# Performance work log

Measured on AMD Instinct MI355X. Metric: run time of the kernel, lower is better.

## Reference

```python
import jax, jax.numpy as jnp
import numpy as np

N = 100000
E = 1600000
IN_FEATS = 512
H1, F1 = 8, 8          # layer1: 8 heads x 8 units
H2, F2 = 1, 40         # layer2: 1 head x out_feats
NEG_SLOPE = 0.2


def setup_inputs() -> dict:
    key = jax.random.key(0)
    ks = jax.random.split(key, 12)
    x = jax.random.normal(ks[0], (N, IN_FEATS), dtype=jnp.float32)
    src = jax.random.randint(ks[1], (E,), 0, N, dtype=jnp.int32)
    dst = jax.random.randint(ks[2], (E,), 0, N, dtype=jnp.int32)
    # Xavier-ish init for params
    W1 = jax.random.normal(ks[3], (IN_FEATS, H1 * F1), dtype=jnp.float32) * (1.0 / np.sqrt(IN_FEATS))
    al1 = jax.random.normal(ks[4], (H1, F1), dtype=jnp.float32) * 0.1
    ar1 = jax.random.normal(ks[5], (H1, F1), dtype=jnp.float32) * 0.1
    b1 = jnp.zeros((H1 * F1,), dtype=jnp.float32)
    W2 = jax.random.normal(ks[6], (H1 * F1, H2 * F2), dtype=jnp.float32) * (1.0 / np.sqrt(H1 * F1))
    al2 = jax.random.normal(ks[7], (H2, F2), dtype=jnp.float32) * 0.1
    ar2 = jax.random.normal(ks[8], (H2, F2), dtype=jnp.float32) * 0.1
    b2 = jnp.zeros((H2 * F2,), dtype=jnp.float32)
    return {"x": x, "src": src, "dst": dst,
            "W1": W1, "al1": al1, "ar1": ar1, "b1": b1,
            "W2": W2, "al2": al2, "ar2": ar2, "b2": b2}


def _gat_conv(feat, src, dst, W, al, ar, b, activation):
    """DGL-style GATConv (dropout disabled / eval mode)."""
    n = feat.shape[0]
    heads, fdim = al.shape
    h = (feat @ W).reshape(n, heads, fdim)            # [N, H, F]
    el = jnp.einsum('nhf,hf->nh', h, al)              # [N, H]
    er = jnp.einsum('nhf,hf->nh', h, ar)              # [N, H]
    e = jax.nn.leaky_relu(el[src] + er[dst], NEG_SLOPE)   # [E, H]
    # edge softmax over incoming edges of each dst node (numerically stable)
    m = jax.ops.segment_max(e, dst, num_segments=n)   # [N, H]
    ex = jnp.exp(e - m[dst])
    s = jax.ops.segment_sum(ex, dst, num_segments=n)  # [N, H]
    alpha = ex / s[dst]                               # [E, H]
    msg = h[src] * alpha[:, :, None]                  # [E, H, F]
    rst = jax.ops.segment_sum(msg, dst, num_segments=n)  # [N, H, F]
    rst = rst + b.reshape(1, heads, fdim)
    if activation is not None:
        rst = activation(rst)
    return rst


def reference(x, src, dst, W1, al1, ar1, b1, W2, al2, ar2, b2):
    h1 = _gat_conv(x, src, dst, W1, al1, ar1, b1, jax.nn.elu)   # [N, H1, F1]
    h1 = h1.reshape(x.shape[0], H1 * F1)                        # flatten(1)
    h2 = _gat_conv(h1, src, dst, W2, al2, ar2, b2, None)        # [N, 1, F2]
    logits = h2.mean(axis=1)                                    # [N, F2]
    return jax.nn.log_softmax(logits, axis=1)
```

## Files before the change

kernel.cpp:

```cpp
#include <hip/hip_runtime.h>
#include <cstdint>
#include <cstddef>

#define IN_F 512
#define C1 64
#define NH 8
#define FD 8
#define C2 40
#define NEG 0.2f

typedef __attribute__((ext_vector_type(8))) short bf16x8;
typedef __attribute__((ext_vector_type(4))) float f32x4;

__device__ inline unsigned short f32_to_bf16_rne(float f) {
    unsigned int u = __float_as_uint(f);
    unsigned int r = (u + 0x7FFFu + ((u >> 16) & 1u)) >> 16;
    return (unsigned short)r;
}
__device__ inline float bf16_to_f32(unsigned short s) {
    return __uint_as_float(((unsigned int)s) << 16);
}

__global__ __launch_bounds__(256) void hist_k(const int* __restrict__ dst, int* __restrict__ deg,
                                              int* __restrict__ pos, int E) {
    int e = blockIdx.x * 256 + threadIdx.x;
    if (e < E) pos[e] = atomicAdd(&deg[dst[e]], 1);
}

__global__ __launch_bounds__(1024) void scan_local_k(const int* __restrict__ deg, int* __restrict__ rowp,
                                                     int* __restrict__ bsums, int n) {
    __shared__ int tmp[1024];
    int tx = threadIdx.x;
    int i = blockIdx.x * 1024 + tx;
    int v = (i < n) ? deg[i] : 0;
    tmp[tx] = v;
    __syncthreads();
    for (int d = 1; d < 1024; d <<= 1) {
        int t = (tx >= d) ? tmp[tx - d] : 0;
        __syncthreads();
        tmp[tx] += t;
        __syncthreads();
    }
    if (i < n) rowp[i] = tmp[tx] - v;
    if (tx == 1023) bsums[blockIdx.x] = tmp[tx];
}

__global__ __launch_bounds__(128) void scan_sums_k(int* bsums, int nb) {
    __shared__ int tmp[128];
    int tx = threadIdx.x;
    int v = (tx < nb) ? bsums[tx] : 0;
    tmp[tx] = v;
    __syncthreads();
    for (int d = 1; d < 128; d <<= 1) {
        int t = (tx >= d) ? tmp[tx - d] : 0;
        __syncthreads();
        tmp[tx] += t;
        __syncthreads();
    }
    if (tx < nb) bsums[tx] = tmp[tx] - v;
}

__global__ __launch_bounds__(1024) void scan_add_k(int* rowp, const int* __restrict__ bsums, int n) {
    int i = blockIdx.x * 1024 + threadIdx.x;
    if (i < n) rowp[i] += bsums[blockIdx.x];
}

__global__ __launch_bounds__(256) void scatter_k(const int* __restrict__ src, const int* __restrict__ dst,
                                                 const int* __restrict__ rowp, const int* __restrict__ pos,
                                                 int* __restrict__ csr_src, int E) {
    int e = blockIdx.x * 256 + threadIdx.x;
    if (e >= E) return;
    csr_src[rowp[dst[e]] + pos[e]] = src[e];
}

__global__ __launch_bounds__(256) void wt_pre_k(const float* __restrict__ W1,
                                                unsigned short* __restrict__ wt_hi,
                                                unsigned short* __restrict__ wt_lo) {
    int id = blockIdx.x * 256 + threadIdx.x;
    if (id >= IN_F * C1) return;
    int col = id & (C1 - 1);
    int k = id >> 6;
    float w = W1[id];
    unsigned short hb = f32_to_bf16_rne(w);
    unsigned short lb = f32_to_bf16_rne(w - bf16_to_f32(hb));
    wt_hi[(size_t)col * IN_F + k] = hb;
    wt_lo[(size_t)col * IN_F + k] = lb;
}

__global__ __launch_bounds__(256) void gemm1_mfma_k(const float* __restrict__ x,
                                                    const unsigned short* __restrict__ wt_hi,
                                                    const unsigned short* __restrict__ wt_lo,
                                                    unsigned short* __restrict__ hb_out, int N) {
    __shared__ alignas(16) unsigned short wlds[2][8192];
    const int tid = threadIdx.x;
    const int wave = tid >> 6, lane = tid & 63;
    const int m = lane & 15, q = lane >> 4;
    const int row = blockIdx.x * 64 + wave * 16 + m;
    const int row_c = row < N ? row : N - 1;
    const float* xp = x + (size_t)row_c * IN_F + q * 8;

    f32x4 acc[4];
#pragma unroll
    for (int ct = 0; ct < 4; ct++) acc[ct] = (f32x4){0.f, 0.f, 0.f, 0.f};
    float4 xr[2][4];

#define WLOAD(c, buf)                                                                              \
    {                                                                                              \
        _Pragma("unroll") for (int j_ = 0; j_ < 4; j_++) {                                         \
            int slot_ = j_ * 256 + wave * 64 + lane;                                               \
            const unsigned short* gbase_ = (slot_ < 512) ? wt_hi : wt_lo;                          \
            int s_ = slot_ & 511;                                                                  \
            int col_ = s_ & 63, kq_ = s_ >> 6;                                                     \
            const unsigned short* g_ = gbase_ + (size_t)col_ * IN_F + (c) * 64 + kq_ * 8;          \
            unsigned short* l_ = &wlds[buf][0] + (size_t)(j_ * 256 + wave * 64) * 8;               \
            __builtin_amdgcn_global_load_lds((const __attribute__((address_space(1))) unsigned int*)g_, \
                                             (__attribute__((address_space(3))) unsigned int*)l_,  \
                                             16, 0, 0);                                            \
        }                                                                                          \
    }
#define XLOAD(c, r)                                  \
    {                                                \
        const float* xsrc_ = xp + (c) * 64;          \
        (r)[0] = *(const float4*)(xsrc_);            \
        (r)[1] = *(const float4*)(xsrc_ + 4);        \
        (r)[2] = *(const float4*)(xsrc_ + 32);       \
        (r)[3] = *(const float4*)(xsrc_ + 36);       \
    }

    WLOAD(0, 0);
    XLOAD(0, xr[0]);

    for (int c = 0; c < 8; c++) {
        int p = c & 1;
        __syncthreads();
        if (c < 7) {
            WLOAD(c + 1, p ^ 1);
            XLOAD(c + 1, xr[p ^ 1]);
        }
#pragma unroll
        for (int ki = 0; ki < 2; ki++) {
            float f[8];
            f[0] = xr[p][ki * 2].x; f[1] = xr[p][ki * 2].y; f[2] = xr[p][ki * 2].z; f[3] = xr[p][ki * 2].w;
            f[4] = xr[p][ki * 2 + 1].x; f[5] = xr[p][ki * 2 + 1].y; f[6] = xr[p][ki * 2 + 1].z; f[7] = xr[p][ki * 2 + 1].w;
            unsigned int u[8], lu[8];
#pragma unroll
            for (int j = 0; j < 8; j++) u[j] = __float_as_uint(f[j]);
            union { uint4 u4; bf16x8 v; } H, L;
            H.u4.x = __builtin_amdgcn_perm(u[1], u[0], 0x07060302u);
            H.u4.y = __builtin_amdgcn_perm(u[3], u[2], 0x07060302u);
            H.u4.z = __builtin_amdgcn_perm(u[5], u[4], 0x07060302u);
            H.u4.w = __builtin_amdgcn_perm(u[7], u[6], 0x07060302u);
#pragma unroll
            for (int j = 0; j < 8; j++)
                lu[j] = __float_as_uint(f[j] - __uint_as_float(u[j] & 0xFFFF0000u));
            L.u4.x = __builtin_amdgcn_perm(lu[1], lu[0], 0x07060302u);
            L.u4.y = __builtin_amdgcn_perm(lu[3], lu[2], 0x07060302u);
            L.u4.z = __builtin_amdgcn_perm(lu[5], lu[4], 0x07060302u);
            L.u4.w = __builtin_amdgcn_perm(lu[7], lu[6], 0x07060302u);
            int kq = ki * 4 + q;
#pragma unroll
            for (int ct = 0; ct < 4; ct++) {
                int slot = kq * 64 + ct * 16 + m;
                bf16x8 bh = *(const bf16x8*)&wlds[p][slot * 8];
                bf16x8 bl = *(const bf16x8*)&wlds[p][4096 + slot * 8];
                acc[ct] = __builtin_amdgcn_mfma_f32_16x16x32_bf16(H.v, bh, acc[ct], 0, 0, 0);
                acc[ct] = __builtin_amdgcn_mfma_f32_16x16x32_bf16(L.v, bh, acc[ct], 0, 0, 0);
                acc[ct] = __builtin_amdgcn_mfma_f32_16x16x32_bf16(H.v, bl, acc[ct], 0, 0, 0);
            }
        }
    }
    int rbase = blockIdx.x * 64 + wave * 16 + q * 4;
#pragma unroll
    for (int r = 0; r < 4; r++) {
        int ro = rbase + r;
        if (ro < N) {
#pragma unroll
            for (int ct = 0; ct < 4; ct++)
                hb_out[(size_t)ro * C1 + ct * 16 + m] = f32_to_bf16_rne(acc[ct][r]);
        }
    }
#undef WLOAD
#undef XLOAD
}

__global__ __launch_bounds__(256) void attn1_k(const unsigned short* __restrict__ hb,
                                               const float* __restrict__ al, const float* __restrict__ ar,
                                               float* __restrict__ el, float* __restrict__ er, int N) {
    int idx = blockIdx.x * 256 + threadIdx.x;
    if (idx >= N * NH) return;
    int n = idx >> 3, hd = idx & 7;
    bf16x8 v = *(const bf16x8*)(hb + (size_t)n * C1 + hd * FD);
    const float4* alp = (const float4*)(al + hd * FD);
    const float4* arp = (const float4*)(ar + hd * FD);
    float4 a0 = alp[0], a1 = alp[1];
    float4 r0 = arp[0], r1 = arp[1];
    float f[8];
#pragma unroll
    for (int j = 0; j < 8; j++) f[j] = bf16_to_f32((unsigned short)v[j]);
    float e_l = f[0] * a0.x + f[1] * a0.y + f[2] * a0.z + f[3] * a0.w +
                f[4] * a1.x + f[5] * a1.y + f[6] * a1.z + f[7] * a1.w;
    float e_r = f[0] * r0.x + f[1] * r0.y + f[2] * r0.z + f[3] * r0.w +
                f[4] * r1.x + f[5] * r1.y + f[6] * r1.z + f[7] * r1.w;
    el[idx] = e_l;
    er[idx] = e_r;
}

__global__ __launch_bounds__(256) void l1_wave_k(const unsigned short* __restrict__ hb,
                                                 const float* __restrict__ el, const float* __restrict__ er,
                                                 const int* __restrict__ rowp, const int* __restrict__ deg,
                                                 const int* __restrict__ csr_src, const float* __restrict__ b1,
                                                 float* __restrict__ h1out, int N) {
    int n = (blockIdx.x * 256 + threadIdx.x) >> 6;
    if (n >= N) return;
    int lane = threadIdx.x & 63;
    int hg = lane >> 3;
    int start = rowp[n], cnt = deg[n];
    float erd = er[n * NH + hg];
    float acc = 0.f, s = 0.f;
    int i = 0;
    for (; i + 4 <= cnt; i += 4) {
        const int* cp = csr_src + start + i;
        int sn0 = cp[0], sn1 = cp[1], sn2 = cp[2], sn3 = cp[3];
        float e0 = el[sn0 * NH + hg];
        float e1 = el[sn1 * NH + hg];
        float e2 = el[sn2 * NH + hg];
        float e3 = el[sn3 * NH + hg];
        unsigned short q0 = hb[(size_t)sn0 * C1 + lane];
        unsigned short q1 = hb[(size_t)sn1 * C1 + lane];
        unsigned short q2 = hb[(size_t)sn2 * C1 + lane];
        unsigned short q3 = hb[(size_t)sn3 * C1 + lane];
        e0 += erd; e1 += erd; e2 += erd; e3 += erd;
        e0 = e0 > 0.f ? e0 : NEG * e0;
        e1 = e1 > 0.f ? e1 : NEG * e1;
        e2 = e2 > 0.f ? e2 : NEG * e2;
        e3 = e3 > 0.f ? e3 : NEG * e3;
        float w0 = __expf(e0), w1 = __expf(e1), w2 = __expf(e2), w3 = __expf(e3);
        s += (w0 + w1) + (w2 + w3);
        acc += w0 * bf16_to_f32(q0) + w1 * bf16_to_f32(q1) + w2 * bf16_to_f32(q2) + w3 * bf16_to_f32(q3);
    }
    for (; i < cnt; i++) {
        int sn = csr_src[start + i];
        float e = el[sn * NH + hg] + erd;
        e = e > 0.f ? e : NEG * e;
        float w0 = __expf(e);
        s += w0;
        acc += w0 * bf16_to_f32(hb[(size_t)sn * C1 + lane]);
    }
    float sinv = (s > 0.f) ? 1.f / s : 0.f;
    float o = acc * sinv + b1[lane];
    o = o > 0.f ? o : (__expf(o) - 1.f);
    h1out[(size_t)n * C1 + lane] = o;
}

__global__ __launch_bounds__(256) void gemm2_attn2_k(const float* __restrict__ h1, const float* __restrict__ W2,
                                                     const float* __restrict__ al2, const float* __restrict__ ar2,
                                                     unsigned short* __restrict__ h2b, float* __restrict__ el2,
                                                     float* __restrict__ er2, int N) {
    __shared__ float ws[C1 * C2];
    __shared__ float hs[64][C1];
    __shared__ float h2s[64][C2];
    __shared__ float a2s[2 * C2];
    int t = threadIdx.x;
    int n0 = blockIdx.x * 64;
    for (int i = t; i < C1 * C2; i += 256) ws[i] = W2[i];
    if (t < C2) a2s[t] = al2[t];
    else if (t < 2 * C2) a2s[t] = ar2[t - C2];
    for (int i = t; i < 64 * 16; i += 256) {
        int r = i >> 4, c4 = i & 15;
        int n = n0 + r;
        float4 v = (n < N) ? *(const float4*)(h1 + (size_t)n * C1 + c4 * 4) : make_float4(0.f, 0.f, 0.f, 0.f);
        *(float4*)&hs[r][c4 * 4] = v;
    }
    __syncthreads();
    for (int o = t; o < 64 * C2; o += 256) {
        int r = o / C2, c = o % C2;
        float sum = 0.f;
#pragma unroll
        for (int k = 0; k < C1; k++) sum += hs[r][k] * ws[k * C2 + c];
        h2s[r][c] = sum;
    }
    __syncthreads();
    for (int o = t; o < 64 * 64; o += 256) {
        int r = o >> 6, c = o & 63;
        int nn = n0 + r;
        if (nn < N) h2b[(size_t)nn * 64 + c] = (c < C2) ? f32_to_bf16_rne(h2s[r][c]) : (unsigned short)0;
    }
    if (t < 64) {
        int nn = n0 + t;
        if (nn < N) {
            float e_l = 0.f, e_r = 0.f;
#pragma unroll
            for (int c = 0; c < C2; c++) {
                float v = h2s[t][c];
                e_l += v * a2s[c];
                e_r += v * a2s[C2 + c];
            }
            el2[nn] = e_l;
            er2[nn] = e_r;
        }
    }
}

__global__ __launch_bounds__(256) void l2_fused_k(const unsigned short* __restrict__ h2b,
                                                  const float* __restrict__ el, const float* __restrict__ er,
                                                  const int* __restrict__ rowp, const int* __restrict__ deg,
                                                  const int* __restrict__ csr_src, const float* __restrict__ b2,
                                                  float* __restrict__ out, int N) {
    int tid = threadIdx.x;
    int n = blockIdx.x * 32 + (tid >> 3);
    int sub = tid & 7;
    if (n >= N) return;
    int start = rowp[n], cnt = deg[n];
    float erd = er[n];
    float s = 0.f;
    float acc[8];
#pragma unroll
    for (int j = 0; j < 8; j++) acc[j] = 0.f;
    int i = 0;
    for (; i + 4 <= cnt; i += 4) {
        const int* cp = csr_src + start + i;
        int sn0 = cp[0], sn1 = cp[1], sn2 = cp[2], sn3 = cp[3];
        float e0 = el[sn0], e1 = el[sn1], e2 = el[sn2], e3 = el[sn3];
        bf16x8 v0 = *(const bf16x8*)(h2b + (size_t)sn0 * 64 + sub * 8);
        bf16x8 v1 = *(const bf16x8*)(h2b + (size_t)sn1 * 64 + sub * 8);
        bf16x8 v2 = *(const bf16x8*)(h2b + (size_t)sn2 * 64 + sub * 8);
        bf16x8 v3 = *(const bf16x8*)(h2b + (size_t)sn3 * 64 + sub * 8);
        e0 += erd; e1 += erd; e2 += erd; e3 += erd;
        e0 = e0 > 0.f ? e0 : NEG * e0;
        e1 = e1 > 0.f ? e1 : NEG * e1;
        e2 = e2 > 0.f ? e2 : NEG * e2;
        e3 = e3 > 0.f ? e3 : NEG * e3;
        float w0 = __expf(e0), w1 = __expf(e1), w2 = __expf(e2), w3 = __expf(e3);
        s += (w0 + w1) + (w2 + w3);
#pragma unroll
        for (int j = 0; j < 8; j++) {
            acc[j] += w0 * bf16_to_f32((unsigned short)v0[j]) + w1 * bf16_to_f32((unsigned short)v1[j]) +
                      w2 * bf16_to_f32((unsigned short)v2[j]) + w3 * bf16_to_f32((unsigned short)v3[j]);
        }
    }
    for (; i < cnt; i++) {
        int sn = csr_src[start + i];
        float e = el[sn] + erd;
        e = e > 0.f ? e : NEG * e;
        float w0 = __expf(e);
        s += w0;
        bf16x8 v = *(const bf16x8*)(h2b + (size_t)sn * 64 + sub * 8);
#pragma unroll
        for (int j = 0; j < 8; j++) acc[j] += w0 * bf16_to_f32((unsigned short)v[j]);
    }
    float sinv = (s > 0.f) ? 1.f / s : 0.f;
    float vals[8];
#pragma unroll
    for (int j = 0; j < 8; j++) {
        int c = sub * 8 + j;
        vals[j] = (c < C2) ? (acc[j] * sinv + b2[c]) : -1e30f;
    }
    float mx = vals[0];
#pragma unroll
    for (int j = 1; j < 8; j++) mx = fmaxf(mx, vals[j]);
#pragma unroll
    for (int off = 1; off < 8; off <<= 1) mx = fmaxf(mx, __shfl_xor(mx, off, 8));
    float se = 0.f;
#pragma unroll
    for (int j = 0; j < 8; j++) se += __expf(vals[j] - mx);
#pragma unroll
    for (int off = 1; off < 8; off <<= 1) se += __shfl_xor(se, off, 8);
    float ls = __logf(se) + mx;
    if (sub < 5) {
        float* op = out + (size_t)n * C2 + sub * 8;
        *(float4*)(op) = make_float4(vals[0] - ls, vals[1] - ls, vals[2] - ls, vals[3] - ls);
        *(float4*)(op + 4) = make_float4(vals[4] - ls, vals[5] - ls, vals[6] - ls, vals[7] - ls);
    }
}

extern "C" void kernel_launch(void* const* d_in, const int* in_sizes, int n_in,
                              void* d_out, int out_size, void* d_ws, size_t ws_size,
                              hipStream_t stream) {
    (void)n_in; (void)out_size; (void)ws_size;
    const float* x   = (const float*)d_in[0];
    const int*   src = (const int*)d_in[1];
    const int*   dst = (const int*)d_in[2];
    const float* W1  = (const float*)d_in[3];
    const float* al1 = (const float*)d_in[4];
    const float* ar1 = (const float*)d_in[5];
    const float* b1  = (const float*)d_in[6];
    const float* W2  = (const float*)d_in[7];
    const float* al2 = (const float*)d_in[8];
    const float* ar2 = (const float*)d_in[9];
    const float* b2  = (const float*)d_in[10];
    float* out = (float*)d_out;
    const int N = in_sizes[0] / IN_F;
    const int E = in_sizes[1];

    char* w = (char*)d_ws;
    auto alloc = [&](size_t bytes) -> char* {
        char* p = w;
        w += (bytes + 255) & ~(size_t)255;
        return p;
    };
    int* deg     = (int*)alloc((size_t)N * 4);
    int* rowp    = (int*)alloc((size_t)N * 4);
    int* bsums   = (int*)alloc(512);
    int* pos     = (int*)alloc((size_t)E * 4);
    int* csr_src = (int*)alloc((size_t)E * 4);
    unsigned short* wt_hi = (unsigned short*)alloc((size_t)IN_F * C1 * 2);
    unsigned short* wt_lo = (unsigned short*)alloc((size_t)IN_F * C1 * 2);
    unsigned short* hb    = (unsigned short*)alloc((size_t)N * C1 * 2);
    float* el1   = (float*)alloc((size_t)N * NH * 4);
    float* er1   = (float*)alloc((size_t)N * NH * 4);
    float* h1    = (float*)alloc((size_t)N * C1 * 4);
    unsigned short* h2b = (unsigned short*)alloc((size_t)N * 64 * 2);
    float* el2   = (float*)alloc((size_t)N * 4);
    float* er2   = (float*)alloc((size_t)N * 4);

    hipMemsetAsync(deg, 0, (size_t)N * 4, stream);

    int ebl = (E + 255) / 256;
    int nb = (N + 1023) / 1024;
    hist_k<<<ebl, 256, 0, stream>>>(dst, deg, pos, E);
    scan_local_k<<<nb, 1024, 0, stream>>>(deg, rowp, bsums, N);
    scan_sums_k<<<1, 128, 0, stream>>>(bsums, nb);
    scan_add_k<<<nb, 1024, 0, stream>>>(rowp, bsums, N);
    scatter_k<<<ebl, 256, 0, stream>>>(src, dst, rowp, pos, csr_src, E);

    wt_pre_k<<<(IN_F * C1 + 255) / 256, 256, 0, stream>>>(W1, wt_hi, wt_lo);
    gemm1_mfma_k<<<(N + 63) / 64, 256, 0, stream>>>(x, wt_hi, wt_lo, hb, N);
    attn1_k<<<(N * NH + 255) / 256, 256, 0, stream>>>(hb, al1, ar1, el1, er1, N);
    l1_wave_k<<<(N * 64 + 255) / 256, 256, 0, stream>>>(hb, el1, er1, rowp, deg, csr_src, b1, h1, N);
    gemm2_attn2_k<<<(N + 63) / 64, 256, 0, stream>>>(h1, W2, al2, ar2, h2b, el2, er2, N);
    l2_fused_k<<<(N + 31) / 32, 256, 0, stream>>>(h2b, el2, er2, rowp, deg, csr_src, b2, out, N);
}
```

Before: 614.0 us.

## Fuse attention logits into GEMM1, two-edge wave gather, compact layer-2 features

```diff
diff --git a/kernel.cpp b/kernel.cpp
--- a/kernel.cpp
+++ b/kernel.cpp
@@ -90,7 +90,9 @@
 __global__ __launch_bounds__(256) void gemm1_mfma_k(const float* __restrict__ x,
                                                     const unsigned short* __restrict__ wt_hi,
                                                     const unsigned short* __restrict__ wt_lo,
-                                                    unsigned short* __restrict__ hb_out, int N) {
+                                                    const float* __restrict__ al, const float* __restrict__ ar,
+                                                    unsigned short* __restrict__ hb_out,
+                                                    float* __restrict__ el, float* __restrict__ er, int N) {
     __shared__ alignas(16) unsigned short wlds[2][8192];
     const int tid = threadIdx.x;
     const int wave = tid >> 6, lane = tid & 63;
@@ -179,30 +181,35 @@
                 hb_out[(size_t)ro * C1 + ct * 16 + m] = f32_to_bf16_rne(acc[ct][r]);
         }
     }
+
+    __syncthreads();
+    float* hst = (float*)&wlds[0][0];
+    {
+        int rr = wave * 16 + q * 4;
+#pragma unroll
+        for (int r = 0; r < 4; r++)
+#pragma unroll
+            for (int ct = 0; ct < 4; ct++)
+                hst[(rr + r) * 69 + ct * 16 + m] = acc[ct][r];
+    }
+    __syncthreads();
+    for (int id = tid; id < 512; id += 256) {
+        int r = id >> 3, hd = id & 7;
+        int nn = blockIdx.x * 64 + r;
+        if (nn < N) {
+            float e_l = 0.f, e_r = 0.f;
+#pragma unroll
+            for (int f = 0; f < 8; f++) {
+                float v = hst[r * 69 + hd * 8 + f];
+                e_l += v * al[hd * 8 + f];
+                e_r += v * ar[hd * 8 + f];
+            }
+            el[(size_t)nn * NH + hd] = e_l;
+            er[(size_t)nn * NH + hd] = e_r;
+        }
+    }
 #undef WLOAD
 #undef XLOAD
-}
-
-__global__ __launch_bounds__(256) void attn1_k(const unsigned short* __restrict__ hb,
-                                               const float* __restrict__ al, const float* __restrict__ ar,
-                                               float* __restrict__ el, float* __restrict__ er, int N) {
-    int idx = blockIdx.x * 256 + threadIdx.x;
-    if (idx >= N * NH) return;
-    int n = idx >> 3, hd = idx & 7;
-    bf16x8 v = *(const bf16x8*)(hb + (size_t)n * C1 + hd * FD);
-    const float4* alp = (const float4*)(al + hd * FD);
-    const float4* arp = (const float4*)(ar + hd * FD);
-    float4 a0 = alp[0], a1 = alp[1];
-    float4 r0 = arp[0], r1 = arp[1];
-    float f[8];
-#pragma unroll
-    for (int j = 0; j < 8; j++) f[j] = bf16_to_f32((unsigned short)v[j]);
-    float e_l = f[0] * a0.x + f[1] * a0.y + f[2] * a0.z + f[3] * a0.w +
-                f[4] * a1.x + f[5] * a1.y + f[6] * a1.z + f[7] * a1.w;
-    float e_r = f[0] * r0.x + f[1] * r0.y + f[2] * r0.z + f[3] * r0.w +
-                f[4] * r1.x + f[5] * r1.y + f[6] * r1.z + f[7] * r1.w;
-    el[idx] = e_l;
-    er[idx] = e_r;
 }
 
 __global__ __launch_bounds__(256) void l1_wave_k(const unsigned short* __restrict__ hb,
@@ -213,43 +220,70 @@
     int n = (blockIdx.x * 256 + threadIdx.x) >> 6;
     if (n >= N) return;
     int lane = threadIdx.x & 63;
-    int hg = lane >> 3;
+    int half = lane >> 5;
+    int fl = lane & 31;
+    int hg = fl >> 2;
     int start = rowp[n], cnt = deg[n];
-    float erd = er[n * NH + hg];
-    float acc = 0.f, s = 0.f;
+    float erd = er[(size_t)n * NH + hg];
+    const unsigned int* hb32 = (const unsigned int*)hb;
+    const int* cp = csr_src + start;
+    float acc0 = 0.f, acc1 = 0.f, s = 0.f;
     int i = 0;
-    for (; i + 4 <= cnt; i += 4) {
-        const int* cp = csr_src + start + i;
-        int sn0 = cp[0], sn1 = cp[1], sn2 = cp[2], sn3 = cp[3];
-        float e0 = el[sn0 * NH + hg];
-        float e1 = el[sn1 * NH + hg];
-        float e2 = el[sn2 * NH + hg];
-        float e3 = el[sn3 * NH + hg];
-        unsigned short q0 = hb[(size_t)sn0 * C1 + lane];
-        unsigned short q1 = hb[(size_t)sn1 * C1 + lane];
-        unsigned short q2 = hb[(size_t)sn2 * C1 + lane];
-        unsigned short q3 = hb[(size_t)sn3 * C1 + lane];
-        e0 += erd; e1 += erd; e2 += erd; e3 += erd;
-        e0 = e0 > 0.f ? e0 : NEG * e0;
-        e1 = e1 > 0.f ? e1 : NEG * e1;
-        e2 = e2 > 0.f ? e2 : NEG * e2;
-        e3 = e3 > 0.f ? e3 : NEG * e3;
-        float w0 = __expf(e0), w1 = __expf(e1), w2 = __expf(e2), w3 = __expf(e3);
-        s += (w0 + w1) + (w2 + w3);
-        acc += w0 * bf16_to_f32(q0) + w1 * bf16_to_f32(q1) + w2 * bf16_to_f32(q2) + w3 * bf16_to_f32(q3);
-    }
-    for (; i < cnt; i++) {
-        int sn = csr_src[start + i];
-        float e = el[sn * NH + hg] + erd;
+    for (; i + 8 <= cnt; i += 8) {
+        int sA = cp[i + half];
+        int sB = cp[i + 2 + half];
+        int sC = cp[i + 4 + half];
+        int sD = cp[i + 6 + half];
+        float eA = el[(size_t)sA * NH + hg];
+        float eB = el[(size_t)sB * NH + hg];
+        float eC = el[(size_t)sC * NH + hg];
+        float eD = el[(size_t)sD * NH + hg];
+        unsigned int qA = hb32[(size_t)sA * 32 + fl];
+        unsigned int qB = hb32[(size_t)sB * 32 + fl];
+        unsigned int qC = hb32[(size_t)sC * 32 + fl];
+        unsigned int qD = hb32[(size_t)sD * 32 + fl];
+        eA += erd; eB += erd; eC += erd; eD += erd;
+        eA = eA > 0.f ? eA : NEG * eA;
+        eB = eB > 0.f ? eB : NEG * eB;
+        eC = eC > 0.f ? eC : NEG * eC;
+        eD = eD > 0.f ? eD : NEG * eD;
+        float wA = __expf(eA), wB = __expf(eB), wC = __expf(eC), wD = __expf(eD);
+        s += (wA + wB) + (wC + wD);
+        acc0 += wA * __uint_as_float(qA << 16) + wB * __uint_as_float(qB << 16) +
+                wC * __uint_as_float(qC << 16) + wD * __uint_as_float(qD << 16);
+        acc1 += wA * __uint_as_float(qA & 0xFFFF0000u) + wB * __uint_as_float(qB & 0xFFFF0000u) +
+                wC * __uint_as_float(qC & 0xFFFF0000u) + wD * __uint_as_float(qD & 0xFFFF0000u);
+    }
+    for (; i + 2 <= cnt; i += 2) {
+        int sn = cp[i + half];
+        float e = el[(size_t)sn * NH + hg] + erd;
         e = e > 0.f ? e : NEG * e;
-        float w0 = __expf(e);
-        s += w0;
-        acc += w0 * bf16_to_f32(hb[(size_t)sn * C1 + lane]);
-    }
+        float w = __expf(e);
+        unsigned int qv = hb32[(size_t)sn * 32 + fl];
+        s += w;
+        acc0 += w * __uint_as_float(qv << 16);
+        acc1 += w * __uint_as_float(qv & 0xFFFF0000u);
+    }
+    if (i < cnt && half == 0) {
+        int sn = cp[i];
+        float e = el[(size_t)sn * NH + hg] + erd;
+        e = e > 0.f ? e : NEG * e;
+        float w = __expf(e);
+        unsigned int qv = hb32[(size_t)sn * 32 + fl];
+        s += w;
+        acc0 += w * __uint_as_float(qv << 16);
+        acc1 += w * __uint_as_float(qv & 0xFFFF0000u);
+    }
+    acc0 += __shfl_xor(acc0, 32);
+    acc1 += __shfl_xor(acc1, 32);
+    s += __shfl_xor(s, 32);
     float sinv = (s > 0.f) ? 1.f / s : 0.f;
-    float o = acc * sinv + b1[lane];
-    o = o > 0.f ? o : (__expf(o) - 1.f);
-    h1out[(size_t)n * C1 + lane] = o;
+    float2 bv = *(const float2*)(b1 + fl * 2);
+    float o0 = acc0 * sinv + bv.x;
+    float o1 = acc1 * sinv + bv.y;
+    o0 = o0 > 0.f ? o0 : (__expf(o0) - 1.f);
+    o1 = o1 > 0.f ? o1 : (__expf(o1) - 1.f);
+    if (half == 0) *(float2*)(h1out + (size_t)n * C1 + fl * 2) = make_float2(o0, o1);
 }
 
 __global__ __launch_bounds__(256) void gemm2_attn2_k(const float* __restrict__ h1, const float* __restrict__ W2,
@@ -280,10 +314,15 @@
         h2s[r][c] = sum;
     }
     __syncthreads();
-    for (int o = t; o < 64 * 64; o += 256) {
-        int r = o >> 6, c = o & 63;
+    unsigned int* h2d = (unsigned int*)h2b;
+    for (int o = t; o < 64 * 20; o += 256) {
+        int r = o / 20, cd = o % 20;
         int nn = n0 + r;
-        if (nn < N) h2b[(size_t)nn * 64 + c] = (c < C2) ? f32_to_bf16_rne(h2s[r][c]) : (unsigned short)0;
+        if (nn < N) {
+            unsigned int lo16 = f32_to_bf16_rne(h2s[r][cd * 2]);
+            unsigned int hi16 = f32_to_bf16_rne(h2s[r][cd * 2 + 1]);
+            h2d[(size_t)nn * 20 + cd] = lo16 | (hi16 << 16);
+        }
     }
     if (t < 64) {
         int nn = n0 + t;
@@ -310,50 +349,53 @@
     int n = blockIdx.x * 32 + (tid >> 3);
     int sub = tid & 7;
     if (n >= N) return;
-    int start = rowp[n], cnt = deg[n];
-    float erd = er[n];
-    float s = 0.f;
-    float acc[8];
-#pragma unroll
-    for (int j = 0; j < 8; j++) acc[j] = 0.f;
-    int i = 0;
-    for (; i + 4 <= cnt; i += 4) {
-        const int* cp = csr_src + start + i;
-        int sn0 = cp[0], sn1 = cp[1], sn2 = cp[2], sn3 = cp[3];
-        float e0 = el[sn0], e1 = el[sn1], e2 = el[sn2], e3 = el[sn3];
-        bf16x8 v0 = *(const bf16x8*)(h2b + (size_t)sn0 * 64 + sub * 8);
-        bf16x8 v1 = *(const bf16x8*)(h2b + (size_t)sn1 * 64 + sub * 8);
-        bf16x8 v2 = *(const bf16x8*)(h2b + (size_t)sn2 * 64 + sub * 8);
-        bf16x8 v3 = *(const bf16x8*)(h2b + (size_t)sn3 * 64 + sub * 8);
-        e0 += erd; e1 += erd; e2 += erd; e3 += erd;
-        e0 = e0 > 0.f ? e0 : NEG * e0;
-        e1 = e1 > 0.f ? e1 : NEG * e1;
-        e2 = e2 > 0.f ? e2 : NEG * e2;
-        e3 = e3 > 0.f ? e3 : NEG * e3;
-        float w0 = __expf(e0), w1 = __expf(e1), w2 = __expf(e2), w3 = __expf(e3);
-        s += (w0 + w1) + (w2 + w3);
-#pragma unroll
-        for (int j = 0; j < 8; j++) {
-            acc[j] += w0 * bf16_to_f32((unsigned short)v0[j]) + w1 * bf16_to_f32((unsigned short)v1[j]) +
-                      w2 * bf16_to_f32((unsigned short)v2[j]) + w3 * bf16_to_f32((unsigned short)v3[j]);
-        }
-    }
-    for (; i < cnt; i++) {
-        int sn = csr_src[start + i];
-        float e = el[sn] + erd;
-        e = e > 0.f ? e : NEG * e;
-        float w0 = __expf(e);
-        s += w0;
-        bf16x8 v = *(const bf16x8*)(h2b + (size_t)sn * 64 + sub * 8);
-#pragma unroll
-        for (int j = 0; j < 8; j++) acc[j] += w0 * bf16_to_f32((unsigned short)v[j]);
-    }
-    float sinv = (s > 0.f) ? 1.f / s : 0.f;
     float vals[8];
-#pragma unroll
-    for (int j = 0; j < 8; j++) {
-        int c = sub * 8 + j;
-        vals[j] = (c < C2) ? (acc[j] * sinv + b2[c]) : -1e30f;
+    if (sub < 5) {
+        int start = rowp[n], cnt = deg[n];
+        float erd = er[n];
+        float s = 0.f;
+        float acc[8];
+#pragma unroll
+        for (int j = 0; j < 8; j++) acc[j] = 0.f;
+        const int* cp = csr_src + start;
+        int i = 0;
+        for (; i + 4 <= cnt; i += 4) {
+            int sn0 = cp[i], sn1 = cp[i + 1], sn2 = cp[i + 2], sn3 = cp[i + 3];
+            float e0 = el[sn0], e1 = el[sn1], e2 = el[sn2], e3 = el[sn3];
+            bf16x8 v0 = *(const bf16x8*)(h2b + (size_t)sn0 * C2 + sub * 8);
+            bf16x8 v1 = *(const bf16x8*)(h2b + (size_t)sn1 * C2 + sub * 8);
+            bf16x8 v2 = *(const bf16x8*)(h2b + (size_t)sn2 * C2 + sub * 8);
+            bf16x8 v3 = *(const bf16x8*)(h2b + (size_t)sn3 * C2 + sub * 8);
+            e0 += erd; e1 += erd; e2 += erd; e3 += erd;
+            e0 = e0 > 0.f ? e0 : NEG * e0;
+            e1 = e1 > 0.f ? e1 : NEG * e1;
+            e2 = e2 > 0.f ? e2 : NEG * e2;
+            e3 = e3 > 0.f ? e3 : NEG * e3;
+            float w0 = __expf(e0), w1 = __expf(e1), w2 = __expf(e2), w3 = __expf(e3);
+            s += (w0 + w1) + (w2 + w3);
+#pragma unroll
+            for (int j = 0; j < 8; j++) {
+                acc[j] += w0 * bf16_to_f32((unsigned short)v0[j]) + w1 * bf16_to_f32((unsigned short)v1[j]) +
+                          w2 * bf16_to_f32((unsigned short)v2[j]) + w3 * bf16_to_f32((unsigned short)v3[j]);
+            }
+        }
+        for (; i < cnt; i++) {
+            int sn = cp[i];
+            float e = el[sn] + erd;
+            e = e > 0.f ? e : NEG * e;
+            float w0 = __expf(e);
+            s += w0;
+            bf16x8 v = *(const bf16x8*)(h2b + (size_t)sn * C2 + sub * 8);
+#pragma unroll
+            for (int j = 0; j < 8; j++) acc[j] += w0 * bf16_to_f32((unsigned short)v[j]);
+        }
+        float sinv = (s > 0.f) ? 1.f / s : 0.f;
+        const float* bp = b2 + sub * 8;
+#pragma unroll
+        for (int j = 0; j < 8; j++) vals[j] = acc[j] * sinv + bp[j];
+    } else {
+#pragma unroll
+        for (int j = 0; j < 8; j++) vals[j] = -1e30f;
     }
     float mx = vals[0];
 #pragma unroll
@@ -409,7 +451,7 @@
     float* el1   = (float*)alloc((size_t)N * NH * 4);
     float* er1   = (float*)alloc((size_t)N * NH * 4);
     float* h1    = (float*)alloc((size_t)N * C1 * 4);
-    unsigned short* h2b = (unsigned short*)alloc((size_t)N * 64 * 2);
+    unsigned short* h2b = (unsigned short*)alloc((size_t)N * C2 * 2);
     float* el2   = (float*)alloc((size_t)N * 4);
     float* er2   = (float*)alloc((size_t)N * 4);
 
@@ -424,8 +466,7 @@
     scatter_k<<<ebl, 256, 0, stream>>>(src, dst, rowp, pos, csr_src, E);
 
     wt_pre_k<<<(IN_F * C1 + 255) / 256, 256, 0, stream>>>(W1, wt_hi, wt_lo);
-    gemm1_mfma_k<<<(N + 63) / 64, 256, 0, stream>>>(x, wt_hi, wt_lo, hb, N);
-    attn1_k<<<(N * NH + 255) / 256, 256, 0, stream>>>(hb, al1, ar1, el1, er1, N);
+    gemm1_mfma_k<<<(N + 63) / 64, 256, 0, stream>>>(x, wt_hi, wt_lo, al1, ar1, hb, el1, er1, N);
     l1_wave_k<<<(N * 64 + 255) / 256, 256, 0, stream>>>(hb, el1, er1, rowp, deg, csr_src, b1, h1, N);
     gemm2_attn2_k<<<(N + 63) / 64, 256, 0, stream>>>(h1, W2, al2, ar2, h2b, el2, er2, N);
     l2_fused_k<<<(N + 31) / 32, 256, 0, stream>>>(h2b, el2, er2, rowp, deg, csr_src, b2, out, N);
```

New measurement: 598.2 us. -2.6%, faster.
